# Optimization experiments

Hardware: AMD Instinct MI355X
Metric: run time of the kernel (lower is better)

Reference implementation:

```python
import jax, jax.numpy as jnp
import numpy as np

N, C_IN, H, W = 32, 16, 256, 256
C_OUT, K = 64, 3

def setup_inputs() -> dict:
    key = jax.random.key(0)
    kx, kw, kb = jax.random.split(key, 3)
    x = jax.random.normal(kx, (N, C_IN, H, W), dtype=jnp.float32)
    # PyTorch Conv2d default init: U(-b, b), b = 1/sqrt(fan_in)
    bound = 1.0 / np.sqrt(C_IN * K * K)
    conv_weight = jax.random.uniform(kw, (C_OUT, C_IN, K, K), minval=-bound, maxval=bound, dtype=jnp.float32)
    conv_bias = jax.random.uniform(kb, (C_OUT,), minval=-bound, maxval=bound, dtype=jnp.float32)
    return {"x": x, "conv_weight": conv_weight, "conv_bias": conv_bias}

def reference(x, conv_weight, conv_bias):
    # conv2d, stride=1, padding=0 (VALID), NCHW / OIHW
    y = jax.lax.conv_general_dilated(
        x, conv_weight,
        window_strides=(1, 1), padding="VALID",
        dimension_numbers=("NCHW", "OIHW", "NCHW"))
    y = y + conv_bias[None, :, None, None]
    # min over output channels (keepdim -> 1 channel), then double tanh
    y = jnp.min(y, axis=1, keepdims=True)  # [N,1,OH,OW]
    return jnp.tanh(jnp.tanh(y))
```

## Files before the change

### kernel.cpp

```cpp
#include <hip/hip_runtime.h>

typedef __bf16 bf16x8 __attribute__((ext_vector_type(8)));
typedef unsigned short us8 __attribute__((ext_vector_type(8)));
typedef unsigned short us2 __attribute__((ext_vector_type(2)));
typedef float f32x16 __attribute__((ext_vector_type(16)));

#define N_IMG 32
#define CI 16
#define HH 256
#define WW 256
#define CO 64
#define OHH 254
#define OWW 254

#define XS_W 258
#define SC 24
#define NSTRIP 24
#define WP_SHORTS (CO * 160)
#define WS_NEEDED ((size_t)WP_SHORTS * 2)

__device__ __forceinline__ unsigned short f2bf(float f) {
  union { float f; unsigned u; } v; v.f = f;
  return (unsigned short)((v.u + 0x7FFFu + ((v.u >> 16) & 1u)) >> 16);
}

#if defined(__has_builtin)
#if __has_builtin(__builtin_amdgcn_cvt_pk_bf16_f32)
#define HAVE_CVT_PK 1
#endif
#endif

__device__ __forceinline__ us2 cvt2(float a, float b) {
#ifdef HAVE_CVT_PK
  typedef __bf16 bf16x2 __attribute__((ext_vector_type(2)));
  bf16x2 r = __builtin_amdgcn_cvt_pk_bf16_f32(a, b);
  return __builtin_bit_cast(us2, r);
#else
  us2 r; r[0] = f2bf(a); r[1] = f2bf(b); return r;
#endif
}

__device__ __forceinline__ float fast_tanh(float x) {
  float cx = fminf(fmaxf(x, -15.f), 15.f);
  float e = __expf(2.f * cx);
  return (e - 1.f) / (e + 1.f);
}

__global__ void prep_w(const float* __restrict__ wg, const float* __restrict__ bg,
                       unsigned short* __restrict__ wp) {
  int idx = blockIdx.x * 256 + threadIdx.x;
  if (idx >= WP_SHORTS) return;
  int oc = idx / 160;
  int k = idx - oc * 160;
  int tap = k >> 4, ci = k & 15;
  float v;
  if (tap < 9)      v = wg[oc * 144 + ci * 9 + tap];
  else if (ci == 0) v = bg[oc];
  else              v = 0.f;
  wp[idx] = f2bf(v);
}

__global__ __launch_bounds__(256, 3)
void conv_fused(const float* __restrict__ xg, const unsigned short* __restrict__ wp,
                float* __restrict__ out) {
  __shared__ __align__(16) unsigned short xs[4 * XS_W * SC];
  const int t = threadIdx.x;
  const int n = blockIdx.x / NSTRIP;
  const int s = blockIdx.x - n * NSTRIP;
  const int oh0 = s * 10 + (s < 14 ? s : 14);
  const int nrows = (s < 14) ? 11 : 10;
  const int oh1 = oh0 + nrows;

  const float* srcT = xg + (size_t)n * (CI * HH * WW) + t;

  {
    float pv[3][16];
#pragma unroll
    for (int r = 0; r < 3; ++r)
#pragma unroll
      for (int j = 0; j < 16; ++j)
        pv[r][j] = srcT[((size_t)j * HH + (oh0 + r)) * WW];
#pragma unroll
    for (int r = 0; r < 3; ++r) {
      union { us8 v8[2]; us2 v2[8]; } pk;
#pragma unroll
      for (int j = 0; j < 8; ++j) pk.v2[j] = cvt2(pv[r][2 * j], pv[r][2 * j + 1]);
      const int slot = (oh0 + r) & 3;
      *(us8*)(xs + (slot * XS_W + t) * SC) = pk.v8[0];
      *(us8*)(xs + (slot * XS_W + t) * SC + 8) = pk.v8[1];
    }
  }
  if (t < 128) {
    const int slot = t >> 5, rem = t & 31;
    xs[(slot * XS_W + 256 + (rem >> 4)) * SC + (rem & 15)] = 0;
  }

  const int lane = t & 63, wave = t >> 6;
  const int lr = lane & 31, qh = lane >> 5;

  const unsigned short* wpl = wp + lr * 160 + qh * 8;
  bf16x8 afrag[2][10];
#pragma unroll
  for (int mt = 0; mt < 2; ++mt)
#pragma unroll
    for (int tap = 0; tap < 10; ++tap)
      afrag[mt][tap] =
          __builtin_bit_cast(bf16x8, *(const us8*)(wpl + mt * 32 * 160 + tap * 16));

  us8 onev = {};
  if (qh == 0) onev[0] = 0x3F80;
  const bf16x8 xone = __builtin_bit_cast(bf16x8, onev);

  const int pb = wave * 64;

  float v[16];
#pragma unroll
  for (int j = 0; j < 16; ++j)
    v[j] = srcT[((size_t)j * HH + (oh0 + 3)) * WW];

  __syncthreads();

  for (int oh = oh0; oh < oh1; ++oh) {
    float vmin[2];
#pragma unroll
    for (int nt = 0; nt < 2; ++nt) {
      f32x16 acc0, acc1;
#pragma unroll
      for (int e = 0; e < 16; ++e) { acc0[e] = 0.f; acc1[e] = 0.f; }
#pragma unroll
      for (int tap = 0; tap < 9; ++tap) {
        const int kh = tap / 3, kw = tap - kh * 3;
        const int slot = (oh + kh) & 3;
        bf16x8 xf = __builtin_bit_cast(
            bf16x8,
            *(const us8*)(xs + (slot * XS_W + pb + nt * 32 + lr + kw) * SC + qh * 8));
        acc0 = __builtin_amdgcn_mfma_f32_32x32x16_bf16(afrag[0][tap], xf, acc0, 0, 0, 0);
        acc1 = __builtin_amdgcn_mfma_f32_32x32x16_bf16(afrag[1][tap], xf, acc1, 0, 0, 0);
      }
      acc0 = __builtin_amdgcn_mfma_f32_32x32x16_bf16(afrag[0][9], xone, acc0, 0, 0, 0);
      acc1 = __builtin_amdgcn_mfma_f32_32x32x16_bf16(afrag[1][9], xone, acc1, 0, 0, 0);

      f32x16 m;
#pragma unroll
      for (int e = 0; e < 16; ++e) m[e] = fminf(acc0[e], acc1[e]);
#pragma unroll
      for (int e = 0; e < 8; ++e) m[e] = fminf(m[e], m[e + 8]);
#pragma unroll
      for (int e = 0; e < 4; ++e) m[e] = fminf(m[e], m[e + 4]);
      float mv = fminf(fminf(m[0], m[1]), fminf(m[2], m[3]));
      mv = fminf(mv, __shfl_xor(mv, 32, 64));
      vmin[nt] = fast_tanh(fast_tanh(mv));
    }

    __builtin_amdgcn_sched_barrier(0);

    if (oh + 1 < oh1) {
      union { us8 v8[2]; us2 v2[8]; } pk;
#pragma unroll
      for (int j = 0; j < 8; ++j) pk.v2[j] = cvt2(v[2 * j], v[2 * j + 1]);
      const int slot = (oh + 3) & 3;
      *(us8*)(xs + (slot * XS_W + t) * SC) = pk.v8[0];
      *(us8*)(xs + (slot * XS_W + t) * SC + 8) = pk.v8[1];
    }

    if (oh + 2 < oh1) {
#pragma unroll
      for (int j = 0; j < 16; ++j)
        v[j] = srcT[((size_t)j * HH + (oh + 4)) * WW];
    }

    const float res = (lane < 32) ? vmin[0] : vmin[1];
    const int ow = pb + lane;
    if (ow < OWW) out[((size_t)n * OHH + oh) * OWW + ow] = res;

    __syncthreads();
  }
}

#define XS_C 24
#define WS_K 168
__global__ __launch_bounds__(256, 2)
void conv_min_tanh(const float* __restrict__ xg, const float* __restrict__ wg,
                   const float* __restrict__ bg, float* __restrict__ out) {
  __shared__ __align__(16) unsigned short xs[3 * XS_W * XS_C];
  __shared__ __align__(16) unsigned short ws[CO * WS_K];
  const int t = threadIdx.x;
  const int n = blockIdx.x / OHH;
  const int oh = blockIdx.x % OHH;
#pragma unroll
  for (int i = 0; i < 36; ++i) {
    int f = i * 256 + t;
    int oc = f / 144;
    int r = f - oc * 144;
    int ci = r / 9;
    int tap = r - ci * 9;
    ws[oc * WS_K + tap * 16 + ci] = f2bf(wg[f]);
  }
  if (t < CO) ws[t * WS_K + 144] = f2bf(bg[t]);
  for (int i = t; i < CO * 15; i += 256) {
    int oc = i / 15;
    ws[oc * WS_K + 145 + (i - oc * 15)] = 0;
  }
  {
    const size_t base_n = (size_t)n * CI * HH * WW;
#pragma unroll
    for (int kh = 0; kh < 3; ++kh) {
#pragma unroll
      for (int half = 0; half < 2; ++half) {
        float v[8];
#pragma unroll
        for (int j = 0; j < 8; ++j) {
          int ci = half * 8 + j;
          v[j] = xg[base_n + ((size_t)ci * HH + (oh + kh)) * WW + t];
        }
        us8 pk;
#pragma unroll
        for (int j = 0; j < 8; ++j) pk[j] = f2bf(v[j]);
        *(us8*)(xs + (kh * XS_W + t) * XS_C + half * 8) = pk;
      }
    }
  }
  if (t < 96) {
    int kh = t >> 5;
    int rem = t & 31;
    int w = 256 + (rem >> 4);
    int ci = rem & 15;
    xs[(kh * XS_W + w) * XS_C + ci] = 0;
  }
  __syncthreads();
  const int lane = t & 63, wave = t >> 6;
  const int lr = lane & 31, qh = lane >> 5;
  bf16x8 afrag[2][10];
#pragma unroll
  for (int mt = 0; mt < 2; ++mt) {
    const unsigned short* wq = ws + (mt * 32 + lr) * WS_K + qh * 8;
#pragma unroll
    for (int tap = 0; tap < 10; ++tap)
      afrag[mt][tap] = __builtin_bit_cast(bf16x8, *(const us8*)(wq + tap * 16));
  }
  f32x16 acc[2][2];
#pragma unroll
  for (int a = 0; a < 2; ++a)
#pragma unroll
    for (int b = 0; b < 2; ++b)
#pragma unroll
      for (int e = 0; e < 16; ++e) acc[a][b][e] = 0.f;
  const unsigned short* xq = xs + (wave * 64 + lr) * XS_C + qh * 8;
#pragma unroll
  for (int tap = 0; tap < 9; ++tap) {
    const int kh = tap / 3, kw = tap - kh * 3;
#pragma unroll
    for (int nt = 0; nt < 2; ++nt) {
      bf16x8 xf = __builtin_bit_cast(
          bf16x8, *(const us8*)(xq + (kh * XS_W + nt * 32 + kw) * XS_C));
      acc[0][nt] = __builtin_amdgcn_mfma_f32_32x32x16_bf16(afrag[0][tap], xf,
                                                           acc[0][nt], 0, 0, 0);
      acc[1][nt] = __builtin_amdgcn_mfma_f32_32x32x16_bf16(afrag[1][tap], xf,
                                                           acc[1][nt], 0, 0, 0);
    }
  }
  {
    us8 one = {};
    if (qh == 0) one[0] = 0x3F80;
    bf16x8 xone = __builtin_bit_cast(bf16x8, one);
#pragma unroll
    for (int nt = 0; nt < 2; ++nt) {
      acc[0][nt] = __builtin_amdgcn_mfma_f32_32x32x16_bf16(afrag[0][9], xone,
                                                           acc[0][nt], 0, 0, 0);
      acc[1][nt] = __builtin_amdgcn_mfma_f32_32x32x16_bf16(afrag[1][9], xone,
                                                           acc[1][nt], 0, 0, 0);
    }
  }
  float vmin[2];
#pragma unroll
  for (int nt = 0; nt < 2; ++nt) {
    float v = acc[0][nt][0];
#pragma unroll
    for (int e = 1; e < 16; ++e) v = fminf(v, acc[0][nt][e]);
#pragma unroll
    for (int e = 0; e < 16; ++e) v = fminf(v, acc[1][nt][e]);
    v = fminf(v, __shfl_xor(v, 32, 64));
    vmin[nt] = fast_tanh(fast_tanh(v));
  }
  float res = (lane < 32) ? vmin[0] : vmin[1];
  int ow = wave * 64 + lane;
  if (ow < OWW) out[((size_t)n * OHH + oh) * OWW + ow] = res;
}

extern "C" void kernel_launch(void* const* d_in, const int* in_sizes, int n_in,
                              void* d_out, int out_size, void* d_ws, size_t ws_size,
                              hipStream_t stream) {
  const float* x = (const float*)d_in[0];
  const float* w = (const float*)d_in[1];
  const float* b = (const float*)d_in[2];
  float* out = (float*)d_out;
  if (ws_size >= WS_NEEDED) {
    unsigned short* wp = (unsigned short*)d_ws;
    prep_w<<<dim3((WP_SHORTS + 255) / 256), dim3(256), 0, stream>>>(w, b, wp);
    conv_fused<<<dim3(N_IMG * NSTRIP), dim3(256), 0, stream>>>(x, wp, out);
  } else {
    conv_min_tanh<<<dim3(N_IMG * OHH), dim3(256), 0, stream>>>(x, w, b, out);
  }
}
```

Measured before the change: 208.3 us.

## Pre-convert input to NHWC bf16 in workspace before fused conv

```diff
diff --git a/kernel.cpp b/kernel.cpp
--- a/kernel.cpp
+++ b/kernel.cpp
@@ -17,7 +17,9 @@
 #define SC 24
 #define NSTRIP 24
 #define WP_SHORTS (CO * 160)
-#define WS_NEEDED ((size_t)WP_SHORTS * 2)
+#define XT_OFF_SHORTS 32768
+#define XT_SHORTS ((size_t)N_IMG * HH * WW * CI)
+#define WS_NEEDED (((size_t)XT_OFF_SHORTS + XT_SHORTS) * 2)
 
 __device__ __forceinline__ unsigned short f2bf(float f) {
   union { float f; unsigned u; } v; v.f = f;
@@ -60,9 +62,25 @@
   wp[idx] = f2bf(v);
 }
 
+__global__ __launch_bounds__(256)
+void nhwc_cvt(const float* __restrict__ xg, unsigned short* __restrict__ xt) {
+  const int b = blockIdx.x;
+  const int t = threadIdx.x;
+  const float* src = xg + (size_t)(b >> 8) * (CI * HH * WW) + (size_t)(b & 255) * WW + t;
+  float v[16];
+#pragma unroll
+  for (int j = 0; j < 16; ++j) v[j] = src[(size_t)j * (HH * WW)];
+  union { us8 v8[2]; us2 v2[8]; } pk;
+#pragma unroll
+  for (int j = 0; j < 8; ++j) pk.v2[j] = cvt2(v[2 * j], v[2 * j + 1]);
+  unsigned short* dst = xt + ((size_t)b * WW + t) * 16;
+  *(us8*)dst = pk.v8[0];
+  *(us8*)(dst + 8) = pk.v8[1];
+}
+
 __global__ __launch_bounds__(256, 3)
-void conv_fused(const float* __restrict__ xg, const unsigned short* __restrict__ wp,
-                float* __restrict__ out) {
+void conv_fused(const unsigned short* __restrict__ xt,
+                const unsigned short* __restrict__ wp, float* __restrict__ out) {
   __shared__ __align__(16) unsigned short xs[4 * XS_W * SC];
   const int t = threadIdx.x;
   const int n = blockIdx.x / NSTRIP;
@@ -71,23 +89,17 @@
   const int nrows = (s < 14) ? 11 : 10;
   const int oh1 = oh0 + nrows;
 
-  const float* srcT = xg + (size_t)n * (CI * HH * WW) + t;
+  const unsigned short* srcC = xt + ((size_t)n * HH * WW + t) * 16;
 
   {
-    float pv[3][16];
-#pragma unroll
-    for (int r = 0; r < 3; ++r)
-#pragma unroll
-      for (int j = 0; j < 16; ++j)
-        pv[r][j] = srcT[((size_t)j * HH + (oh0 + r)) * WW];
 #pragma unroll
     for (int r = 0; r < 3; ++r) {
-      union { us8 v8[2]; us2 v2[8]; } pk;
-#pragma unroll
-      for (int j = 0; j < 8; ++j) pk.v2[j] = cvt2(pv[r][2 * j], pv[r][2 * j + 1]);
+      const unsigned short* p = srcC + (size_t)(oh0 + r) * (WW * 16);
+      us8 a = *(const us8*)p;
+      us8 b = *(const us8*)(p + 8);
       const int slot = (oh0 + r) & 3;
-      *(us8*)(xs + (slot * XS_W + t) * SC) = pk.v8[0];
-      *(us8*)(xs + (slot * XS_W + t) * SC + 8) = pk.v8[1];
+      *(us8*)(xs + (slot * XS_W + t) * SC) = a;
+      *(us8*)(xs + (slot * XS_W + t) * SC + 8) = b;
     }
   }
   if (t < 128) {
@@ -113,10 +125,12 @@
 
   const int pb = wave * 64;
 
-  float v[16];
-#pragma unroll
-  for (int j = 0; j < 16; ++j)
-    v[j] = srcT[((size_t)j * HH + (oh0 + 3)) * WW];
+  us8 va, vb;
+  {
+    const unsigned short* p = srcC + (size_t)(oh0 + 3) * (WW * 16);
+    va = *(const us8*)p;
+    vb = *(const us8*)(p + 8);
+  }
 
   __syncthreads();
 
@@ -155,18 +169,15 @@
     __builtin_amdgcn_sched_barrier(0);
 
     if (oh + 1 < oh1) {
-      union { us8 v8[2]; us2 v2[8]; } pk;
-#pragma unroll
-      for (int j = 0; j < 8; ++j) pk.v2[j] = cvt2(v[2 * j], v[2 * j + 1]);
       const int slot = (oh + 3) & 3;
-      *(us8*)(xs + (slot * XS_W + t) * SC) = pk.v8[0];
-      *(us8*)(xs + (slot * XS_W + t) * SC + 8) = pk.v8[1];
+      *(us8*)(xs + (slot * XS_W + t) * SC) = va;
+      *(us8*)(xs + (slot * XS_W + t) * SC + 8) = vb;
     }
 
     if (oh + 2 < oh1) {
-#pragma unroll
-      for (int j = 0; j < 16; ++j)
-        v[j] = srcT[((size_t)j * HH + (oh + 4)) * WW];
+      const unsigned short* p = srcC + (size_t)(oh + 4) * (WW * 16);
+      va = *(const us8*)p;
+      vb = *(const us8*)(p + 8);
     }
 
     const float res = (lane < 32) ? vmin[0] : vmin[1];
@@ -296,8 +307,10 @@
   float* out = (float*)d_out;
   if (ws_size >= WS_NEEDED) {
     unsigned short* wp = (unsigned short*)d_ws;
+    unsigned short* xt = (unsigned short*)d_ws + XT_OFF_SHORTS;
     prep_w<<<dim3((WP_SHORTS + 255) / 256), dim3(256), 0, stream>>>(w, b, wp);
-    conv_fused<<<dim3(N_IMG * NSTRIP), dim3(256), 0, stream>>>(x, wp, out);
+    nhwc_cvt<<<dim3(N_IMG * HH), dim3(256), 0, stream>>>(x, xt);
+    conv_fused<<<dim3(N_IMG * NSTRIP), dim3(256), 0, stream>>>(xt, wp, out);
   } else {
     conv_min_tanh<<<dim3(N_IMG * OHH), dim3(256), 0, stream>>>(x, w, b, out);
   }
```

After: 237.8 us. +14.2%, slower.

## Split output channels across 512-thread blocks and reduce min via shared memory

Applied to the files above, without the earlier changes.

```diff
diff --git a/kernel.cpp b/kernel.cpp
--- a/kernel.cpp
+++ b/kernel.cpp
@@ -15,7 +15,7 @@
 
 #define XS_W 258
 #define SC 24
-#define NSTRIP 24
+#define NSTRIP 16
 #define WP_SHORTS (CO * 160)
 #define WS_NEEDED ((size_t)WP_SHORTS * 2)
 
@@ -60,35 +60,32 @@
   wp[idx] = f2bf(v);
 }
 
-__global__ __launch_bounds__(256, 3)
+__global__ __launch_bounds__(512, 4)
 void conv_fused(const float* __restrict__ xg, const unsigned short* __restrict__ wp,
                 float* __restrict__ out) {
   __shared__ __align__(16) unsigned short xs[4 * XS_W * SC];
+  __shared__ float pmin[2][2][256];
   const int t = threadIdx.x;
   const int n = blockIdx.x / NSTRIP;
   const int s = blockIdx.x - n * NSTRIP;
-  const int oh0 = s * 10 + (s < 14 ? s : 14);
-  const int nrows = (s < 14) ? 11 : 10;
+  const int oh0 = (s < 14) ? 16 * s : 224 + 15 * (s - 14);
+  const int nrows = (s < 14) ? 16 : 15;
   const int oh1 = oh0 + nrows;
 
-  const float* srcT = xg + (size_t)n * (CI * HH * WW) + t;
-
-  {
-    float pv[3][16];
-#pragma unroll
-    for (int r = 0; r < 3; ++r)
-#pragma unroll
-      for (int j = 0; j < 16; ++j)
-        pv[r][j] = srcT[((size_t)j * HH + (oh0 + r)) * WW];
-#pragma unroll
-    for (int r = 0; r < 3; ++r) {
-      union { us8 v8[2]; us2 v2[8]; } pk;
-#pragma unroll
-      for (int j = 0; j < 8; ++j) pk.v2[j] = cvt2(pv[r][2 * j], pv[r][2 * j + 1]);
-      const int slot = (oh0 + r) & 3;
-      *(us8*)(xs + (slot * XS_W + t) * SC) = pk.v8[0];
-      *(us8*)(xs + (slot * XS_W + t) * SC + 8) = pk.v8[1];
-    }
+  const int w = t & 255, half = t >> 8;
+  const float* srcT =
+      xg + (size_t)n * (CI * HH * WW) + (size_t)(half * 8) * (HH * WW) + w;
+
+#pragma unroll
+  for (int r = 0; r < 3; ++r) {
+    float v[8];
+#pragma unroll
+    for (int j = 0; j < 8; ++j) v[j] = srcT[((size_t)j * HH + (oh0 + r)) * WW];
+    union { us8 v8; us2 v2[4]; } pk;
+#pragma unroll
+    for (int j = 0; j < 4; ++j) pk.v2[j] = cvt2(v[2 * j], v[2 * j + 1]);
+    const int slot = (oh0 + r) & 3;
+    *(us8*)(xs + (slot * XS_W + w) * SC + half * 8) = pk.v8;
   }
   if (t < 128) {
     const int slot = t >> 5, rem = t & 31;
@@ -97,36 +94,33 @@
 
   const int lane = t & 63, wave = t >> 6;
   const int lr = lane & 31, qh = lane >> 5;
-
-  const unsigned short* wpl = wp + lr * 160 + qh * 8;
-  bf16x8 afrag[2][10];
-#pragma unroll
-  for (int mt = 0; mt < 2; ++mt)
-#pragma unroll
-    for (int tap = 0; tap < 10; ++tap)
-      afrag[mt][tap] =
-          __builtin_bit_cast(bf16x8, *(const us8*)(wpl + mt * 32 * 160 + tap * 16));
+  const int mt = wave >> 2;
+  const int pb = (wave & 3) * 64;
+
+  const unsigned short* wpl = wp + (mt * 32 + lr) * 160 + qh * 8;
+  bf16x8 afrag[10];
+#pragma unroll
+  for (int tap = 0; tap < 10; ++tap)
+    afrag[tap] = __builtin_bit_cast(bf16x8, *(const us8*)(wpl + tap * 16));
 
   us8 onev = {};
   if (qh == 0) onev[0] = 0x3F80;
   const bf16x8 xone = __builtin_bit_cast(bf16x8, onev);
 
-  const int pb = wave * 64;
-
-  float v[16];
-#pragma unroll
-  for (int j = 0; j < 16; ++j)
-    v[j] = srcT[((size_t)j * HH + (oh0 + 3)) * WW];
+  float v[8];
+#pragma unroll
+  for (int j = 0; j < 8; ++j) v[j] = srcT[((size_t)j * HH + (oh0 + 3)) * WW];
 
   __syncthreads();
 
   for (int oh = oh0; oh < oh1; ++oh) {
-    float vmin[2];
+    const int par = oh & 1;
+
 #pragma unroll
     for (int nt = 0; nt < 2; ++nt) {
-      f32x16 acc0, acc1;
-#pragma unroll
-      for (int e = 0; e < 16; ++e) { acc0[e] = 0.f; acc1[e] = 0.f; }
+      f32x16 acc;
+#pragma unroll
+      for (int e = 0; e < 16; ++e) acc[e] = 0.f;
 #pragma unroll
       for (int tap = 0; tap < 9; ++tap) {
         const int kh = tap / 3, kw = tap - kh * 3;
@@ -134,46 +128,42 @@
         bf16x8 xf = __builtin_bit_cast(
             bf16x8,
             *(const us8*)(xs + (slot * XS_W + pb + nt * 32 + lr + kw) * SC + qh * 8));
-        acc0 = __builtin_amdgcn_mfma_f32_32x32x16_bf16(afrag[0][tap], xf, acc0, 0, 0, 0);
-        acc1 = __builtin_amdgcn_mfma_f32_32x32x16_bf16(afrag[1][tap], xf, acc1, 0, 0, 0);
+        acc = __builtin_amdgcn_mfma_f32_32x32x16_bf16(afrag[tap], xf, acc, 0, 0, 0);
       }
-      acc0 = __builtin_amdgcn_mfma_f32_32x32x16_bf16(afrag[0][9], xone, acc0, 0, 0, 0);
-      acc1 = __builtin_amdgcn_mfma_f32_32x32x16_bf16(afrag[1][9], xone, acc1, 0, 0, 0);
-
-      f32x16 m;
-#pragma unroll
-      for (int e = 0; e < 16; ++e) m[e] = fminf(acc0[e], acc1[e]);
+      acc = __builtin_amdgcn_mfma_f32_32x32x16_bf16(afrag[9], xone, acc, 0, 0, 0);
+
+      f32x16 m = acc;
 #pragma unroll
       for (int e = 0; e < 8; ++e) m[e] = fminf(m[e], m[e + 8]);
 #pragma unroll
       for (int e = 0; e < 4; ++e) m[e] = fminf(m[e], m[e + 4]);
       float mv = fminf(fminf(m[0], m[1]), fminf(m[2], m[3]));
       mv = fminf(mv, __shfl_xor(mv, 32, 64));
-      vmin[nt] = fast_tanh(fast_tanh(mv));
-    }
-
-    __builtin_amdgcn_sched_barrier(0);
+      if (lane < 32) pmin[par][mt][pb + nt * 32 + lane] = mv;
+    }
 
     if (oh + 1 < oh1) {
-      union { us8 v8[2]; us2 v2[8]; } pk;
-#pragma unroll
-      for (int j = 0; j < 8; ++j) pk.v2[j] = cvt2(v[2 * j], v[2 * j + 1]);
+      union { us8 v8; us2 v2[4]; } pk;
+#pragma unroll
+      for (int j = 0; j < 4; ++j) pk.v2[j] = cvt2(v[2 * j], v[2 * j + 1]);
       const int slot = (oh + 3) & 3;
-      *(us8*)(xs + (slot * XS_W + t) * SC) = pk.v8[0];
-      *(us8*)(xs + (slot * XS_W + t) * SC + 8) = pk.v8[1];
+      *(us8*)(xs + (slot * XS_W + w) * SC + half * 8) = pk.v8;
     }
 
     if (oh + 2 < oh1) {
 #pragma unroll
-      for (int j = 0; j < 16; ++j)
-        v[j] = srcT[((size_t)j * HH + (oh + 4)) * WW];
-    }
-
-    const float res = (lane < 32) ? vmin[0] : vmin[1];
-    const int ow = pb + lane;
-    if (ow < OWW) out[((size_t)n * OHH + oh) * OWW + ow] = res;
+      for (int j = 0; j < 8; ++j) v[j] = srcT[((size_t)j * HH + (oh + 4)) * WW];
+    }
 
     __syncthreads();
+
+    if (mt == 0) {
+      const float a = pmin[par][0][pb + lane];
+      const float b = pmin[par][1][pb + lane];
+      const float r = fast_tanh(fast_tanh(fminf(a, b)));
+      const int ow = pb + lane;
+      if (ow < OWW) out[((size_t)n * OHH + oh) * OWW + ow] = r;
+    }
   }
 }
 
@@ -297,7 +287,7 @@
   if (ws_size >= WS_NEEDED) {
     unsigned short* wp = (unsigned short*)d_ws;
     prep_w<<<dim3((WP_SHORTS + 255) / 256), dim3(256), 0, stream>>>(w, b, wp);
-    conv_fused<<<dim3(N_IMG * NSTRIP), dim3(256), 0, stream>>>(x, wp, out);
+    conv_fused<<<dim3(N_IMG * NSTRIP), dim3(512), 0, stream>>>(x, wp, out);
   } else {
     conv_min_tanh<<<dim3(N_IMG * OHH), dim3(256), 0, stream>>>(x, w, b, out);
   }
```

Measured after the change: 209.7 us. No clear change (+0.7%).
